# Kernel tuning notes

Measured on AMD Instinct MI355X. Metric: run time of the kernel, lower is better.

## Reference

```python
import jax, jax.numpy as jnp
import numpy as np

N_LAYERS = 2
DIN = 128
DOUT = 128


def _uniform(key, shape, std):
    return jax.random.uniform(key, shape, jnp.float32, -std, std)


def setup_inputs() -> dict:
    key = jax.random.key(0)
    ks = jax.random.split(key, 12)
    B, T, N, F = 2, 8, 10000, DIN
    E = 320000
    x = jax.random.normal(ks[0], (B, T, N, F), jnp.float32)
    edge_index = jax.random.randint(ks[1], (2, E), 0, N, jnp.int64)
    edge_weight = jax.random.uniform(ks[2], (E,), jnp.float32)
    std_w = 1.0 / np.sqrt(DOUT)
    std_p = 1.0 / np.sqrt(DIN)
    std_g = 1.0 / np.sqrt(DIN)  # torch GRUCell init: U(-1/sqrt(H), 1/sqrt(H))
    W0 = _uniform(ks[3], (N_LAYERS, DIN, DOUT), std_w)
    p = _uniform(ks[4], (N_LAYERS, DIN, 1), std_p)
    w_ih = _uniform(ks[5], (N_LAYERS, 3 * DIN, DIN), std_g)
    w_hh = _uniform(ks[6], (N_LAYERS, 3 * DIN, DIN), std_g)
    b_ih = _uniform(ks[7], (N_LAYERS, 3 * DIN), std_g)
    b_hh = _uniform(ks[8], (N_LAYERS, 3 * DIN), std_g)
    bias = jnp.zeros((N_LAYERS, DOUT), jnp.float32)
    return {"x": x, "edge_index": edge_index, "edge_weight": edge_weight,
            "W0": W0, "p": p, "w_ih": w_ih, "w_hh": w_hh,
            "b_ih": b_ih, "b_hh": b_hh, "bias": bias}


def _gru_cell(xg, hg, wih, whh, bih, bhh):
    # torch.nn.GRUCell: gate order r, z, n
    gi = xg @ wih.T + bih
    gh = hg @ whh.T + bhh
    ir, iz, inn = jnp.split(gi, 3, axis=-1)
    hr, hz, hn = jnp.split(gh, 3, axis=-1)
    r = jax.nn.sigmoid(ir + hr)
    z = jax.nn.sigmoid(iz + hz)
    n = jnp.tanh(inn + r * hn)
    return (1.0 - z) * n + z * hg


def _topk_pool(xb, pc, k):
    # xb: [b, N, din], pc: [din, 1] -> [b, k, din]
    scores = (xb @ pc)[..., 0] / jnp.linalg.norm(pc)  # [b, N]
    vals, idx = jax.lax.top_k(scores, k)               # [b, k], sorted desc
    g = jnp.take_along_axis(xb, idx[..., None], axis=1)  # [b, k, din]
    return g * jnp.tanh(vals)[..., None]


def reference(x, edge_index, edge_weight, W0, p, w_ih, w_hh, b_ih, b_hh, bias):
    B, T, N, F = x.shape
    dout = W0.shape[-1]
    # --- GCN symmetric normalization with self-loops (done once, static graph) ---
    src, tgt = edge_index[0], edge_index[1]
    loops = jnp.arange(N, dtype=src.dtype)
    row = jnp.concatenate([src, loops])
    col = jnp.concatenate([tgt, loops])
    w = jnp.concatenate([edge_weight, jnp.ones((N,), x.dtype)])
    deg = jnp.zeros((N,), x.dtype).at[col].add(w)
    dinv = jnp.where(deg > 0, deg ** -0.5, 0.0)
    wn = dinv[row] * w * dinv[col]  # [E+N]

    def step(Ws, xt):
        out = xt  # [b, N, din]
        new_Ws = []
        for c in range(N_LAYERS):
            W = Ws[c]  # [b, din, dout]
            din = W.shape[1]
            pooled = _topk_pool(out, p[c], dout)                 # [b, dout, din]
            hg = W.transpose(0, 2, 1).reshape(B * dout, din)     # (b dout) din
            xg = pooled.reshape(B * dout, din)
            hg = _gru_cell(xg, hg, w_ih[c], w_hh[c], b_ih[c], b_hh[c])
            W = hg.reshape(B, dout, din).transpose(0, 2, 1)      # [b, din, dout]
            o = jnp.einsum('bnd,bde->bne', out, W)               # [b, N, dout]
            # gather-scale-scatter propagation (aggr='add')
            m = o[:, row, :] * wn[None, :, None]                 # [b, E+N, dout]
            o = jnp.zeros((B, N, dout), x.dtype).at[:, col, :].add(m)
            o = o + bias[c]
            out = jax.nn.relu(o)
            new_Ws.append(W)
        return tuple(new_Ws), out

    Ws0 = tuple(jnp.broadcast_to(W0[c], (B,) + W0[c].shape) for c in range(N_LAYERS))
    _, outs = jax.lax.scan(step, Ws0, jnp.moveaxis(x, 1, 0))
    return outs[-1]  # output at final step, [b, N, hidden]
```

## Files before the change

### kernel.cpp

```cpp
#include <hip/hip_runtime.h>
#include <hip/hip_bf16.h>
#include <math.h>


#define BB 2
#define TT 8
#define FF 128
#define GG 384
#define BINS 8192
#define CAP 512

typedef float v4f __attribute__((ext_vector_type(4)));

__device__ __forceinline__ float bf2f(unsigned short u) {
  return __uint_as_float((unsigned)u << 16);
}
__device__ __forceinline__ unsigned short f2bf(float f) {
  unsigned x = __float_as_uint(f);
  unsigned r = ((x >> 16) & 1u) + 0x7fffu;
  return (unsigned short)((x + r) >> 16);
}
__device__ __forceinline__ float4 bf4(ushort4 u) {
  return make_float4(bf2f(u.x), bf2f(u.y), bf2f(u.z), bf2f(u.w));
}

__global__ void prep_kernel(const int* __restrict__ ei32, int E, int* __restrict__ flag,
                            const float* __restrict__ p, float* __restrict__ pinv) {
  if (blockIdx.x == 0) {
    int step = E / 256;
    int e = threadIdx.x * step;
    if (ei32[2 * e + 1] != 0) *flag = 1;
  } else {
    int c = blockIdx.x - 1, tid = threadIdx.x;
    float s = 0.f;
    if (tid < 128) { float v = p[c * FF + tid]; s = v * v; }
    for (int o = 32; o; o >>= 1) s += __shfl_xor(s, o, 64);
    __shared__ float red[4];
    if ((tid & 63) == 0) red[tid >> 6] = s;
    __syncthreads();
    if (tid == 0) pinv[c] = 1.0f / sqrtf(red[0] + red[1] + red[2] + red[3]);
  }
}

__device__ __forceinline__ void edge_fetch(const void* ei, int is32, int E,
                                           int e, const float* ew,
                                           int& row, int& col, float& w) {
  if (e < E) {
    if (is32) {
      const int* p = (const int*)ei;
      row = p[e]; col = p[E + e];
    } else {
      const long long* p = (const long long*)ei;
      row = (int)p[e]; col = (int)p[(long long)E + e];
    }
    w = ew[e];
  } else {
    row = col = e - E; w = 1.0f;
  }
}

__global__ void hist_kernel(const void* ei, const int* flag, int E, int N,
                            const float* __restrict__ ew,
                            float* __restrict__ deg, int* __restrict__ counts) {
  int e = blockIdx.x * 256 + threadIdx.x;
  if (e >= E + N) return;
  int row, col; float w;
  edge_fetch(ei, *flag, E, e, ew, row, col, w);
  atomicAdd(&deg[col], w);
  atomicAdd(&counts[col], 1);
}

__global__ __launch_bounds__(1024) void scan_kernel(
    const int* __restrict__ counts, const float* __restrict__ deg,
    int* __restrict__ offsets, float* __restrict__ dinv, int N, int EN) {
  __shared__ int wtot[16];
  int tid = threadIdx.x, lane = tid & 63, wid = tid >> 6;
  int base = tid * 10;
  int lc[10]; int s10 = 0;
#pragma unroll
  for (int q = 0; q < 10; ++q) {
    int idx = base + q;
    int cv = (idx < N) ? counts[idx] : 0;
    lc[q] = cv; s10 += cv;
    if (idx < N) {
      float d = deg[idx];
      dinv[idx] = (d > 0.f) ? 1.0f / sqrtf(d) : 0.f;
    }
  }
  int s = s10;
#pragma unroll
  for (int off = 1; off <= 32; off <<= 1) {
    int v = __shfl_up(s, off, 64);
    if (lane >= off) s += v;
  }
  if (lane == 63) wtot[wid] = s;
  __syncthreads();
  int pre = 0;
  for (int w2 = 0; w2 < wid; ++w2) pre += wtot[w2];
  int run = pre + s - s10;
#pragma unroll
  for (int q = 0; q < 10; ++q) {
    int idx = base + q;
    if (idx < N) { offsets[idx] = run; run += lc[q]; }
  }
  if (tid == 0) offsets[N] = EN;
}

__global__ void scatter_kernel(const void* ei, const int* flag, int E, int N,
                               const float* __restrict__ ew,
                               const float* __restrict__ dinv,
                               const int* __restrict__ offs,
                               int* __restrict__ cursors,
                               int2* __restrict__ ep) {
  int e = blockIdx.x * 256 + threadIdx.x;
  if (e >= E + N) return;
  int row, col; float w;
  edge_fetch(ei, *flag, E, e, ew, row, col, w);
  int pos = atomicAdd(&cursors[col], 1);
  ep[offs[col] + pos] = make_int2(row, __float_as_int(dinv[row] * w * dinv[col]));
}

template <int SRC_BF16>
__global__ __launch_bounds__(256) void prop_kernel(
    const void* __restrict__ srcv, size_t s_tstride, size_t s_bstride,
    float* __restrict__ dst, size_t d_tstride, size_t d_bstride,
    const int2* __restrict__ ep, const int* __restrict__ offs,
    const float* __restrict__ p, const float* __restrict__ pinv,
    unsigned long long* __restrict__ keys, int* __restrict__ hist, int N) {
  int t = blockIdx.y;
  int lane = threadIdx.x & 63;
  int half = lane >> 5, sub = lane & 31;
  int v = blockIdx.x * 4 + (threadIdx.x >> 6);
  if (v >= N) return;
  int e0 = offs[v], e1 = offs[v + 1];
  size_t o0 = (size_t)t * s_tstride, o1 = o0 + s_bstride;
  const float4* f0 = (const float4*)srcv + (o0 >> 2);
  const float4* f1 = (const float4*)srcv + (o1 >> 2);
  const ushort4* u0 = (const ushort4*)srcv + (o0 >> 2);
  const ushort4* u1 = (const ushort4*)srcv + (o1 >> 2);
  float4 acc0 = {0.f, 0.f, 0.f, 0.f}, acc1 = {0.f, 0.f, 0.f, 0.f};
  for (int base = e0; base < e1; base += 64) {
    int cnt = e1 - base; if (cnt > 64) cnt = 64;
    int2 m = make_int2(0, 0);
    if (lane < cnt) m = ep[base + lane];
    for (int i = 0; i < cnt; i += 4) {
      int i0 = i + half, i1 = i + 2 + half;
      int sA = __shfl(m.x, i0, 64);
      float wA = __int_as_float(__shfl(m.y, i0, 64));
      int sB = __shfl(m.x, i1, 64);
      float wB = __int_as_float(__shfl(m.y, i1, 64));
      if (i0 >= cnt) wA = 0.f;
      if (i1 >= cnt) wB = 0.f;
      size_t rA = (size_t)sA * 32 + sub, rB = (size_t)sB * 32 + sub;
      float4 a0, a1, b0, b1;
      if constexpr (SRC_BF16) {
        a0 = bf4(u0[rA]); a1 = bf4(u1[rA]);
        b0 = bf4(u0[rB]); b1 = bf4(u1[rB]);
      } else {
        a0 = f0[rA]; a1 = f1[rA];
        b0 = f0[rB]; b1 = f1[rB];
      }
      acc0.x += wA * a0.x + wB * b0.x;  acc0.y += wA * a0.y + wB * b0.y;
      acc0.z += wA * a0.z + wB * b0.z;  acc0.w += wA * a0.w + wB * b0.w;
      acc1.x += wA * a1.x + wB * b1.x;  acc1.y += wA * a1.y + wB * b1.y;
      acc1.z += wA * a1.z + wB * b1.z;  acc1.w += wA * a1.w + wB * b1.w;
    }
  }
  acc0.x += __shfl_xor(acc0.x, 32, 64); acc0.y += __shfl_xor(acc0.y, 32, 64);
  acc0.z += __shfl_xor(acc0.z, 32, 64); acc0.w += __shfl_xor(acc0.w, 32, 64);
  acc1.x += __shfl_xor(acc1.x, 32, 64); acc1.y += __shfl_xor(acc1.y, 32, 64);
  acc1.z += __shfl_xor(acc1.z, 32, 64); acc1.w += __shfl_xor(acc1.w, 32, 64);
  if (half == 0) {
    v4f* d0 = (v4f*)((float4*)(dst + (size_t)t * d_tstride) +
                     (size_t)v * 32 + sub);
    v4f* d1 = (v4f*)((float4*)(dst + (size_t)t * d_tstride + d_bstride) +
                     (size_t)v * 32 + sub);
    v4f s0 = {acc0.x, acc0.y, acc0.z, acc0.w};
    v4f s1 = {acc1.x, acc1.y, acc1.z, acc1.w};
    __builtin_nontemporal_store(s0, d0);
    __builtin_nontemporal_store(s1, d1);
  }
  if constexpr (!SRC_BF16) {
    if (p) {
      float4 xv = (half ? f1 : f0)[(size_t)v * 32 + sub];
      float4 pp = ((const float4*)p)[sub];
      float sc = xv.x * pp.x + xv.y * pp.y + xv.z * pp.z + xv.w * pp.w;
#pragma unroll
      for (int o = 1; o <= 16; o <<= 1) sc += __shfl_xor(sc, o, 64);
      if (sub == 0) {
        float ss = sc * (*pinv);
        unsigned u = __float_as_uint(ss);
        u = (u & 0x80000000u) ? ~u : (u | 0x80000000u);
        int tb = t * 2 + half;
        keys[(size_t)tb * N + v] = ((unsigned long long)u << 32) | (unsigned)(~v);
        atomicAdd(&hist[tb * BINS + (u >> 19)], 1);
      }
    }
  }
}

__device__ __forceinline__ unsigned long long shfl_xor_u64(unsigned long long x,
                                                           int m) {
  unsigned lo = (unsigned)x, hi = (unsigned)(x >> 32);
  lo = __shfl_xor(lo, m, 64);
  hi = __shfl_xor(hi, m, 64);
  return ((unsigned long long)hi << 32) | lo;
}

__global__ __launch_bounds__(1024) void selectsort_kernel(
    const unsigned long long* __restrict__ keys, const int* __restrict__ hist,
    int N, int* __restrict__ idx_sel, float* __restrict__ gate_sel) {
  int tb = blockIdx.y * 2 + blockIdx.x, tid = threadIdx.x;
  int lane = tid & 63, wid = tid >> 6;
  const int* h = hist + tb * BINS;
  __shared__ int wtot[16];
  __shared__ unsigned long long cand[CAP];
  __shared__ int sT, ncnt;
  int base = tid * 8;
  int lc[8]; int local = 0;
#pragma unroll
  for (int q = 0; q < 8; ++q) { lc[q] = h[base + q]; local += lc[q]; }
  if (tid == 0) ncnt = 0;
  int s = local;
#pragma unroll
  for (int off = 1; off <= 32; off <<= 1) {
    int v = __shfl_down(s, off, 64);
    if (lane + off < 64) s += v;
  }
  if (lane == 0) wtot[wid] = s;
  __syncthreads();
  int above_w = 0;
  for (int w2 = wid + 1; w2 < 16; ++w2) above_w += wtot[w2];
  int incl = above_w + s;
  int above = incl - local;
  if (above < 128 && incl >= 128) {
    int cnt = above;
#pragma unroll
    for (int q = 7; q >= 0; --q) {
      int c = lc[q];
      if (cnt + c >= 128) { sT = base + q; break; }
      cnt += c;
    }
  }
  __syncthreads();
  int T = sT;
  for (int i = tid; i < N; i += 1024) {
    unsigned long long kk = keys[(size_t)tb * N + i];
    if ((int)(kk >> 51) >= T) {
      int pos = atomicAdd(&ncnt, 1);
      if (pos < CAP) cand[pos] = kk;
    }
  }
  __syncthreads();
  if (tid < 64) {
    int nc = ncnt < CAP ? ncnt : CAP;
    unsigned long long v[8];
#pragma unroll
    for (int r = 0; r < 8; ++r) {
      int e = r * 64 + lane;
      v[r] = (e < nc) ? cand[e] : 0ULL;
    }
    for (int k = 2; k <= 512; k <<= 1)
      for (int j = k >> 1; j > 0; j >>= 1) {
        if (j >= 64) {
          int rj = j >> 6;
#pragma unroll
          for (int r = 0; r < 8; ++r)
            if (!(r & rj)) {
              int r2 = r | rj;
              bool up = (((r * 64) & k) != 0);
              unsigned long long a = v[r], c = v[r2];
              bool sw = up ? (a > c) : (a < c);
              if (sw) { v[r] = c; v[r2] = a; }
            }
        } else {
#pragma unroll
          for (int r = 0; r < 8; ++r) {
            unsigned long long o = shfl_xor_u64(v[r], j);
            int e = r * 64 + lane;
            bool up = (e & k) != 0;
            bool lower = (lane & j) == 0;
            unsigned long long mn = v[r] < o ? v[r] : o;
            unsigned long long mx = v[r] < o ? o : v[r];
            v[r] = (lower == up) ? mn : mx;
          }
        }
      }
#pragma unroll
    for (int r = 0; r < 2; ++r) {
      int e = r * 64 + lane;
      unsigned long long kk = v[r];
      unsigned n = ~((unsigned)kk);
      unsigned u = (unsigned)(kk >> 32);
      float sc = (u & 0x80000000u) ? __uint_as_float(u & 0x7FFFFFFFu)
                                   : __uint_as_float(~u);
      idx_sel[tb * 128 + e] = (int)n;
      gate_sel[tb * 128 + e] = tanhf(sc);
    }
  }
}

template <int SRC_BF16>
__global__ __launch_bounds__(256) void wchain_kernel(
    const void* __restrict__ srcv, size_t src_tstride, size_t src_bstride,
    const int* __restrict__ idx_sel, const float* __restrict__ gate_sel,
    const float* __restrict__ Winit,
    const float* __restrict__ wih, const float* __restrict__ whh,
    const float* __restrict__ bih, const float* __restrict__ bhh,
    float* __restrict__ snap) {
  int b = blockIdx.x, j0 = blockIdx.y * 4;
  int tid = threadIdx.x, side = tid >> 7, kl = tid & 127;
  __shared__ float pooled[4][FF];
  __shared__ float hbuf[4][FF];
  __shared__ float ghbuf[3][4][FF];
  for (int e = tid; e < 4 * FF; e += 256) {
    int j = e >> 7, m = e & 127;
    hbuf[j][m] = Winit[m * FF + j0 + j];
  }
  float b0 = side ? bhh[kl] : bih[kl];
  float b1 = side ? bhh[FF + kl] : bih[FF + kl];
  float b2 = side ? bhh[2 * FF + kl] : bih[2 * FF + kl];
  const float* wmat = side ? whh : wih;
  const float4* w0p = (const float4*)(wmat + (size_t)(0 * FF + kl) * FF);
  const float4* w1p = (const float4*)(wmat + (size_t)(1 * FF + kl) * FF);
  const float4* w2p = (const float4*)(wmat + (size_t)(2 * FF + kl) * FF);
  for (int t = 0; t < TT; ++t) {
    int tb = t * 2 + b;
    __syncthreads();
    for (int e = tid; e < 4 * FF; e += 256) {
      int j = e >> 7, m = e & 127;
      int n = idx_sel[tb * 128 + j0 + j];
      float g = gate_sel[tb * 128 + j0 + j];
      size_t off = (size_t)t * src_tstride + (size_t)b * src_bstride +
                   (size_t)n * FF + m;
      float xv;
      if constexpr (SRC_BF16) xv = bf2f(((const unsigned short*)srcv)[off]);
      else                    xv = ((const float*)srcv)[off];
      pooled[j][m] = xv * g;
    }
    __syncthreads();
    const float4* vsrc = (const float4*)(side ? &hbuf[0][0] : &pooled[0][0]);
    float acc0[4] = {}, acc1[4] = {}, acc2[4] = {};
    for (int mq = 0; mq < 32; ++mq) {
      float4 w0 = w0p[mq], w1 = w1p[mq], w2 = w2p[mq];
#pragma unroll
      for (int j = 0; j < 4; ++j) {
        float4 v = vsrc[j * 32 + mq];
        acc0[j] += v.x * w0.x + v.y * w0.y + v.z * w0.z + v.w * w0.w;
        acc1[j] += v.x * w1.x + v.y * w1.y + v.z * w1.z + v.w * w1.w;
        acc2[j] += v.x * w2.x + v.y * w2.y + v.z * w2.z + v.w * w2.w;
      }
    }
    if (side) {
#pragma unroll
      for (int j = 0; j < 4; ++j) {
        ghbuf[0][j][kl] = acc0[j] + b0;
        ghbuf[1][j][kl] = acc1[j] + b1;
        ghbuf[2][j][kl] = acc2[j] + b2;
      }
    }
    __syncthreads();
    if (!side) {
#pragma unroll
      for (int j = 0; j < 4; ++j) {
        float rr = 1.0f / (1.0f + expf(-(acc0[j] + b0 + ghbuf[0][j][kl])));
        float zz = 1.0f / (1.0f + expf(-(acc1[j] + b1 + ghbuf[1][j][kl])));
        float nn = tanhf(acc2[j] + b2 + rr * ghbuf[2][j][kl]);
        float h = hbuf[j][kl];
        float hn = (1.0f - zz) * nn + zz * h;
        hbuf[j][kl] = hn;
        snap[((size_t)tb * FF + kl) * FF + j0 + j] = hn;
      }
    }
  }
}

__global__ __launch_bounds__(256) void gemm_kernel(
    const float* __restrict__ A, size_t a_tstride, size_t a_bstride,
    const float* __restrict__ Wsnap, const float* __restrict__ bias,
    float* __restrict__ outf, unsigned short* __restrict__ outb,
    size_t o_tstride, size_t o_bstride,
    const float* __restrict__ p1, const float* __restrict__ pinv1,
    unsigned long long* __restrict__ keys, int* __restrict__ hist, int N) {
  int nb = blockIdx.x, b = blockIdx.y, t = blockIdx.z;
  int tb = t * 2 + b;
  __shared__ float Ast[32][132];
  __shared__ float Bs[32][128];
  __shared__ float spart[128][17];
  __shared__ float p1s[128];
  int tid = threadIdx.x;
  int tc = tid & 15, tr = tid >> 4;
  if (p1 && tid < 128) p1s[tid] = p1[tid];
  float acc[8][8] = {};
  const float* Ab = A + (size_t)t * a_tstride + (size_t)b * a_bstride;
  const float* Wb = Wsnap + (size_t)tb * FF * FF;
  for (int kc = 0; kc < 4; ++kc) {
    int k0 = kc * 32;
    __syncthreads();
    for (int e = tid; e < 128 * 32; e += 256) {
      int r = e >> 5, kk = e & 31;
      int n = nb * 128 + r;
      Ast[kk][r] = (n < N) ? Ab[(size_t)n * FF + k0 + kk] : 0.f;
    }
    for (int e = tid; e < 32 * 128; e += 256) {
      int r = e >> 7, dd = e & 127;
      Bs[r][dd] = Wb[(k0 + r) * FF + dd];
    }
    __syncthreads();
#pragma unroll 4
    for (int kk = 0; kk < 32; ++kk) {
      const float4* arow = (const float4*)Ast[kk];
      float4 a0 = arow[tr * 2], a1 = arow[tr * 2 + 1];
      const float4* brow = (const float4*)Bs[kk];
      float4 b0 = brow[tc * 2], b1 = brow[tc * 2 + 1];
      float av[8] = {a0.x, a0.y, a0.z, a0.w, a1.x, a1.y, a1.z, a1.w};
      float bv[8] = {b0.x, b0.y, b0.z, b0.w, b1.x, b1.y, b1.z, b1.w};
#pragma unroll
      for (int i = 0; i < 8; ++i)
#pragma unroll
        for (int j = 0; j < 8; ++j) acc[i][j] += av[i] * bv[j];
    }
  }
  float bb[8];
#pragma unroll
  for (int j = 0; j < 8; ++j) bb[j] = bias[tc * 8 + j];
  size_t obase = (size_t)t * o_tstride + (size_t)b * o_bstride;
#pragma unroll
  for (int i = 0; i < 8; ++i) {
    int n = nb * 128 + tr * 8 + i;
    float v[8]; float part = 0.f;
#pragma unroll
    for (int j = 0; j < 8; ++j) {
      v[j] = fmaxf(acc[i][j] + bb[j], 0.f);
      if (p1) part += v[j] * p1s[tc * 8 + j];
    }
    if (n < N) {
      if (outb) {
        unsigned short* dst = outb + obase + (size_t)n * FF + tc * 8;
        uint4 pk;
        pk.x = (unsigned)f2bf(v[0]) | ((unsigned)f2bf(v[1]) << 16);
        pk.y = (unsigned)f2bf(v[2]) | ((unsigned)f2bf(v[3]) << 16);
        pk.z = (unsigned)f2bf(v[4]) | ((unsigned)f2bf(v[5]) << 16);
        pk.w = (unsigned)f2bf(v[6]) | ((unsigned)f2bf(v[7]) << 16);
        *(uint4*)dst = pk;
      } else {
        float4* dst = (float4*)(outf + obase + (size_t)n * FF + tc * 8);
        dst[0] = make_float4(v[0], v[1], v[2], v[3]);
        dst[1] = make_float4(v[4], v[5], v[6], v[7]);
      }
    }
    if (p1) spart[tr * 8 + i][tc] = part;
  }
  if (p1) {
    __syncthreads();
    if (tid < 128) {
      int n = nb * 128 + tid;
      if (n < N) {
        float s = 0.f;
#pragma unroll
        for (int q = 0; q < 16; ++q) s += spart[tid][q];
        s *= *pinv1;
        unsigned u = __float_as_uint(s);
        u = (u & 0x80000000u) ? ~u : (u | 0x80000000u);
        keys[(size_t)tb * N + n] = ((unsigned long long)u << 32) | (unsigned)(~n);
        atomicAdd(&hist[tb * BINS + (u >> 19)], 1);
      }
    }
  }
}

extern "C" void kernel_launch(void* const* d_in, const int* in_sizes, int n_in,
                              void* d_out, int out_size, void* d_ws, size_t ws_size,
                              hipStream_t stream) {
  const float* x   = (const float*)d_in[0];
  const void*  ei  = d_in[1];
  const float* ew  = (const float*)d_in[2];
  const float* W0  = (const float*)d_in[3];
  const float* p   = (const float*)d_in[4];
  const float* wih = (const float*)d_in[5];
  const float* whh = (const float*)d_in[6];
  const float* bih = (const float*)d_in[7];
  const float* bhh = (const float*)d_in[8];
  const float* bias= (const float*)d_in[9];

  const int E  = in_sizes[2];
  const int N  = in_sizes[0] / (BB * TT * FF);
  const int EN = E + N;
  const size_t NF = (size_t)N * FF;

  char* w = (char*)d_ws;
  auto alloc = [&](size_t bytes) -> char* {
    char* r = w; w += (bytes + 255) & ~(size_t)255; return r;
  };
  char* zbeg = w;
  float* deg      = (float*)alloc((size_t)N * 4);
  int*   counts   = (int*)  alloc((size_t)N * 4);
  int*   cursors  = (int*)  alloc((size_t)N * 4);
  int*   flag     = (int*)  alloc(4);
  int*   hist     = (int*)  alloc((size_t)2 * TT * BB * BINS * 4);
  char* zend = w;
  int*   offsets  = (int*)  alloc((size_t)(N + 1) * 4);
  float* dinv     = (float*)alloc((size_t)N * 4);
  float* pinv     = (float*)alloc(2 * 4);
  int2*  ep       = (int2*) alloc((size_t)EN * 8);
  unsigned long long* keys0 = (unsigned long long*)alloc((size_t)TT * BB * N * 8);
  unsigned long long* keys1 = (unsigned long long*)alloc((size_t)TT * BB * N * 8);
  int*   idx0     = (int*)  alloc((size_t)TT * BB * 128 * 4);
  float* gate0    = (float*)alloc((size_t)TT * BB * 128 * 4);
  int*   idx1     = (int*)  alloc((size_t)TT * BB * 128 * 4);
  float* gate1    = (float*)alloc((size_t)TT * BB * 128 * 4);
  float* W0snap   = (float*)alloc((size_t)TT * BB * FF * FF * 4);
  float* W1snap   = (float*)alloc((size_t)TT * BB * FF * FF * 4);
  float* xp       = (float*)alloc((size_t)TT * BB * NF * 4);
  unsigned short* act0 = (unsigned short*)alloc((size_t)TT * BB * NF * 2);
  float* xq       = (float*)alloc((size_t)BB * NF * 4);
  int* hist0 = hist;
  int* hist1 = hist + (size_t)TT * BB * BINS;

  hipMemsetAsync(zbeg, 0, (size_t)(zend - zbeg), stream);

  prep_kernel<<<3, 256, 0, stream>>>((const int*)ei, E, flag, p, pinv);
  hist_kernel<<<(EN + 255) / 256, 256, 0, stream>>>(ei, flag, E, N, ew, deg, counts);
  scan_kernel<<<1, 1024, 0, stream>>>(counts, deg, offsets, dinv, N, EN);
  scatter_kernel<<<(EN + 255) / 256, 256, 0, stream>>>(ei, flag, E, N, ew, dinv,
                                                       offsets, cursors, ep);

  prop_kernel<0><<<dim3((N + 3) / 4, TT), 256, 0, stream>>>(
      x, NF, (size_t)TT * NF, xp, (size_t)BB * NF, NF,
      ep, offsets, p, pinv, keys0, hist0, N);

  selectsort_kernel<<<dim3(BB, TT), 1024, 0, stream>>>(
      keys0, hist0, N, idx0, gate0);

  wchain_kernel<0><<<dim3(BB, 32), 256, 0, stream>>>(
      x, NF, (size_t)TT * NF, idx0, gate0, W0,
      wih, whh, bih, bhh, W0snap);

  gemm_kernel<<<dim3((N + 127) / 128, BB, TT), 256, 0, stream>>>(
      xp, (size_t)BB * NF, NF, W0snap, bias,
      nullptr, act0, (size_t)BB * NF, NF,
      p + FF, pinv + 1, keys1, hist1, N);

  selectsort_kernel<<<dim3(BB, TT), 1024, 0, stream>>>(
      keys1, hist1, N, idx1, gate1);

  wchain_kernel<1><<<dim3(BB, 32), 256, 0, stream>>>(
      act0, (size_t)BB * NF, NF, idx1, gate1, W0 + FF * FF,
      wih + (size_t)GG * FF, whh + (size_t)GG * FF,
      bih + GG, bhh + GG, W1snap);

  prop_kernel<1><<<dim3((N + 3) / 4, 1), 256, 0, stream>>>(
      act0 + (size_t)(TT - 1) * BB * NF, 0, NF, xq, 0, NF,
      ep, offsets, nullptr, nullptr, nullptr, nullptr, N);

  gemm_kernel<<<dim3((N + 127) / 128, BB, 1), 256, 0, stream>>>(
      xq, 0, NF, W1snap + (size_t)(TT - 1) * BB * FF * FF, bias + FF,
      (float*)d_out, nullptr, 0, NF,
      nullptr, nullptr, nullptr, nullptr, N);
}
```

Measured before the change: 919.3 us.

## Split propagation feature dimension across blocks with t-interleaved grid ordering

The GCN propagation kernel now splits the 128-wide feature row into quarter (fp32) or half (bf16) chunks across separate blocks. Each wave processes 8 edges in parallel with 8 lanes per edge reading 16-byte pieces, replacing the old 2-edge-per-wave shuffle loop. The launch becomes 1D with the time index interleaved in the low bits, so blocks sharing a node run together and gather the same source rows through cache. The intent is more memory-level parallelism and cache reuse for the irregular gathers, at the cost of re-reading edge lists once per feature chunk and a three-step cross-lane reduction.

```diff
diff --git a/kernel.cpp b/kernel.cpp
--- a/kernel.cpp
+++ b/kernel.cpp
@@ -19,9 +19,6 @@
   unsigned x = __float_as_uint(f);
   unsigned r = ((x >> 16) & 1u) + 0x7fffu;
   return (unsigned short)((x + r) >> 16);
-}
-__device__ __forceinline__ float4 bf4(ushort4 u) {
-  return make_float4(bf2f(u.x), bf2f(u.y), bf2f(u.z), bf2f(u.w));
 }
 
 __global__ void prep_kernel(const int* __restrict__ ei32, int E, int* __restrict__ flag,
@@ -126,68 +123,91 @@
     float* __restrict__ dst, size_t d_tstride, size_t d_bstride,
     const int2* __restrict__ ep, const int* __restrict__ offs,
     const float* __restrict__ p, const float* __restrict__ pinv,
-    unsigned long long* __restrict__ keys, int* __restrict__ hist, int N) {
-  int t = blockIdx.y;
+    unsigned long long* __restrict__ keys, int* __restrict__ hist,
+    int N, int NG, int t8) {
+  constexpr int PER = SRC_BF16 ? 8 : 4;
+  constexpr int RSU = SRC_BF16 ? 16 : 32;
+  int lid = blockIdx.x;
+  int t, s;
+  if (t8) { t = lid & 7; s = lid >> 3; } else { t = 0; s = lid; }
+  int fq = s / NG, vg = s - fq * NG;
   int lane = threadIdx.x & 63;
-  int half = lane >> 5, sub = lane & 31;
-  int v = blockIdx.x * 4 + (threadIdx.x >> 6);
+  int e = lane >> 3, sub = lane & 7;
+  int v = vg * 4 + (threadIdx.x >> 6);
   if (v >= N) return;
   int e0 = offs[v], e1 = offs[v + 1];
   size_t o0 = (size_t)t * s_tstride, o1 = o0 + s_bstride;
-  const float4* f0 = (const float4*)srcv + (o0 >> 2);
-  const float4* f1 = (const float4*)srcv + (o1 >> 2);
-  const ushort4* u0 = (const ushort4*)srcv + (o0 >> 2);
-  const ushort4* u1 = (const ushort4*)srcv + (o1 >> 2);
-  float4 acc0 = {0.f, 0.f, 0.f, 0.f}, acc1 = {0.f, 0.f, 0.f, 0.f};
-  for (int base = e0; base < e1; base += 64) {
-    int cnt = e1 - base; if (cnt > 64) cnt = 64;
-    int2 m = make_int2(0, 0);
-    if (lane < cnt) m = ep[base + lane];
-    for (int i = 0; i < cnt; i += 4) {
-      int i0 = i + half, i1 = i + 2 + half;
-      int sA = __shfl(m.x, i0, 64);
-      float wA = __int_as_float(__shfl(m.y, i0, 64));
-      int sB = __shfl(m.x, i1, 64);
-      float wB = __int_as_float(__shfl(m.y, i1, 64));
-      if (i0 >= cnt) wA = 0.f;
-      if (i1 >= cnt) wB = 0.f;
-      size_t rA = (size_t)sA * 32 + sub, rB = (size_t)sB * 32 + sub;
-      float4 a0, a1, b0, b1;
-      if constexpr (SRC_BF16) {
-        a0 = bf4(u0[rA]); a1 = bf4(u1[rA]);
-        b0 = bf4(u0[rB]); b1 = bf4(u1[rB]);
-      } else {
-        a0 = f0[rA]; a1 = f1[rA];
-        b0 = f0[rB]; b1 = f1[rB];
-      }
-      acc0.x += wA * a0.x + wB * b0.x;  acc0.y += wA * a0.y + wB * b0.y;
-      acc0.z += wA * a0.z + wB * b0.z;  acc0.w += wA * a0.w + wB * b0.w;
-      acc1.x += wA * a1.x + wB * b1.x;  acc1.y += wA * a1.y + wB * b1.y;
-      acc1.z += wA * a1.z + wB * b1.z;  acc1.w += wA * a1.w + wB * b1.w;
-    }
-  }
-  acc0.x += __shfl_xor(acc0.x, 32, 64); acc0.y += __shfl_xor(acc0.y, 32, 64);
-  acc0.z += __shfl_xor(acc0.z, 32, 64); acc0.w += __shfl_xor(acc0.w, 32, 64);
-  acc1.x += __shfl_xor(acc1.x, 32, 64); acc1.y += __shfl_xor(acc1.y, 32, 64);
-  acc1.z += __shfl_xor(acc1.z, 32, 64); acc1.w += __shfl_xor(acc1.w, 32, 64);
-  if (half == 0) {
-    v4f* d0 = (v4f*)((float4*)(dst + (size_t)t * d_tstride) +
-                     (size_t)v * 32 + sub);
-    v4f* d1 = (v4f*)((float4*)(dst + (size_t)t * d_tstride + d_bstride) +
-                     (size_t)v * 32 + sub);
-    v4f s0 = {acc0.x, acc0.y, acc0.z, acc0.w};
-    v4f s1 = {acc1.x, acc1.y, acc1.z, acc1.w};
-    __builtin_nontemporal_store(s0, d0);
-    __builtin_nontemporal_store(s1, d1);
+  const uint4* g0;
+  const uint4* g1;
+  if constexpr (SRC_BF16) {
+    g0 = (const uint4*)((const unsigned short*)srcv + o0);
+    g1 = (const uint4*)((const unsigned short*)srcv + o1);
+  } else {
+    g0 = (const uint4*)((const float*)srcv + o0);
+    g1 = (const uint4*)((const float*)srcv + o1);
+  }
+  int fqs = fq * 8;
+  float acc0[PER], acc1[PER];
+#pragma unroll
+  for (int q = 0; q < PER; ++q) { acc0[q] = 0.f; acc1[q] = 0.f; }
+  const long long* epq = (const long long*)ep;
+  for (int i = e0; i < e1; i += 8) {
+    int idx = i + e;
+    bool ok = idx < e1;
+    long long ev = __builtin_nontemporal_load(epq + (ok ? idx : e1 - 1));
+    int row = (int)ev;
+    float wv = ok ? __int_as_float((int)(ev >> 32)) : 0.f;
+    size_t r = (size_t)row * RSU + fqs + sub;
+    uint4 ra = g0[r], rb = g1[r];
+    if constexpr (SRC_BF16) {
+      acc0[0] += wv * bf2f(ra.x & 0xffff); acc0[1] += wv * bf2f(ra.x >> 16);
+      acc0[2] += wv * bf2f(ra.y & 0xffff); acc0[3] += wv * bf2f(ra.y >> 16);
+      acc0[4] += wv * bf2f(ra.z & 0xffff); acc0[5] += wv * bf2f(ra.z >> 16);
+      acc0[6] += wv * bf2f(ra.w & 0xffff); acc0[7] += wv * bf2f(ra.w >> 16);
+      acc1[0] += wv * bf2f(rb.x & 0xffff); acc1[1] += wv * bf2f(rb.x >> 16);
+      acc1[2] += wv * bf2f(rb.y & 0xffff); acc1[3] += wv * bf2f(rb.y >> 16);
+      acc1[4] += wv * bf2f(rb.z & 0xffff); acc1[5] += wv * bf2f(rb.z >> 16);
+      acc1[6] += wv * bf2f(rb.w & 0xffff); acc1[7] += wv * bf2f(rb.w >> 16);
+    } else {
+      acc0[0] += wv * __uint_as_float(ra.x);
+      acc0[1] += wv * __uint_as_float(ra.y);
+      acc0[2] += wv * __uint_as_float(ra.z);
+      acc0[3] += wv * __uint_as_float(ra.w);
+      acc1[0] += wv * __uint_as_float(rb.x);
+      acc1[1] += wv * __uint_as_float(rb.y);
+      acc1[2] += wv * __uint_as_float(rb.z);
+      acc1[3] += wv * __uint_as_float(rb.w);
+    }
+  }
+#pragma unroll
+  for (int mk = 8; mk <= 32; mk <<= 1) {
+#pragma unroll
+    for (int q = 0; q < PER; ++q) {
+      acc0[q] += __shfl_xor(acc0[q], mk, 64);
+      acc1[q] += __shfl_xor(acc1[q], mk, 64);
+    }
+  }
+  if (e < 2) {
+    float* ob = dst + (size_t)t * d_tstride + (e ? d_bstride : 0);
+    float* av = e ? acc1 : acc0;
+    size_t fo = (size_t)v * FF + fq * (PER * 8) + sub * PER;
+    v4f st0 = {av[0], av[1], av[2], av[3]};
+    __builtin_nontemporal_store(st0, (v4f*)(ob + fo));
+    if constexpr (SRC_BF16) {
+      v4f st1 = {av[4], av[5], av[6], av[7]};
+      __builtin_nontemporal_store(st1, (v4f*)(ob + fo + 4));
+    }
   }
   if constexpr (!SRC_BF16) {
-    if (p) {
-      float4 xv = (half ? f1 : f0)[(size_t)v * 32 + sub];
-      float4 pp = ((const float4*)p)[sub];
+    if (p && fq == 0) {
+      int half = lane >> 5, i32 = lane & 31;
+      const v4f* xrow = (const v4f*)(half ? g1 : g0);
+      v4f xv = __builtin_nontemporal_load(xrow + (size_t)v * 32 + i32);
+      float4 pp = ((const float4*)p)[i32];
       float sc = xv.x * pp.x + xv.y * pp.y + xv.z * pp.z + xv.w * pp.w;
 #pragma unroll
       for (int o = 1; o <= 16; o <<= 1) sc += __shfl_xor(sc, o, 64);
-      if (sub == 0) {
+      if (i32 == 0) {
         float ss = sc * (*pinv);
         unsigned u = __float_as_uint(ss);
         u = (u & 0x80000000u) ? ~u : (u | 0x80000000u);
@@ -487,6 +507,7 @@
   const int N  = in_sizes[0] / (BB * TT * FF);
   const int EN = E + N;
   const size_t NF = (size_t)N * FF;
+  const int NG = (N + 3) / 4;
 
   char* w = (char*)d_ws;
   auto alloc = [&](size_t bytes) -> char* {
@@ -525,9 +546,9 @@
   scatter_kernel<<<(EN + 255) / 256, 256, 0, stream>>>(ei, flag, E, N, ew, dinv,
                                                        offsets, cursors, ep);
 
-  prop_kernel<0><<<dim3((N + 3) / 4, TT), 256, 0, stream>>>(
+  prop_kernel<0><<<NG * 4 * TT, 256, 0, stream>>>(
       x, NF, (size_t)TT * NF, xp, (size_t)BB * NF, NF,
-      ep, offsets, p, pinv, keys0, hist0, N);
+      ep, offsets, p, pinv, keys0, hist0, N, NG, 1);
 
   selectsort_kernel<<<dim3(BB, TT), 1024, 0, stream>>>(
       keys0, hist0, N, idx0, gate0);
@@ -549,9 +570,9 @@
       wih + (size_t)GG * FF, whh + (size_t)GG * FF,
       bih + GG, bhh + GG, W1snap);
 
-  prop_kernel<1><<<dim3((N + 3) / 4, 1), 256, 0, stream>>>(
+  prop_kernel<1><<<NG * 2, 256, 0, stream>>>(
       act0 + (size_t)(TT - 1) * BB * NF, 0, NF, xq, 0, NF,
-      ep, offsets, nullptr, nullptr, nullptr, nullptr, N);
+      ep, offsets, nullptr, nullptr, nullptr, nullptr, N, NG, 0);
 
   gemm_kernel<<<dim3((N + 127) / 128, BB, 1), 256, 0, stream>>>(
       xq, 0, NF, W1snap + (size_t)(TT - 1) * BB * FF * FF, bias + FF,
```

Result: no change. 932.6 us (+1.4%).
